# Performance work log

Measured on AMD Instinct MI355X. Metric: run time of the kernel, lower is better.

Reference implementation:

```python
import jax, jax.numpy as jnp
import numpy as np

B, N, DIM, H, DH = 8, 1024, 512, 8, 64
SCALE = DH ** -0.5
EPS = 1e-6


def setup_inputs() -> dict:
    key = jax.random.key(0)
    k1, k2, k3, k4 = jax.random.split(key, 4)
    x = jax.random.normal(k1, (B, N, DIM), dtype=jnp.float32)
    policy = (jax.random.uniform(k2, (B, N, 1)) < 0.7).astype(jnp.float32)
    W_qkv = jax.random.normal(k3, (DIM, 3 * H * DH), dtype=jnp.float32) * 0.02
    W_out = jax.random.normal(k4, (H * DH, DIM), dtype=jnp.float32) * 0.02
    b_out = jnp.zeros((DIM,), dtype=jnp.float32)
    return {"x": x, "policy": policy, "W_qkv": W_qkv, "W_out": W_out, "b_out": b_out}


def _softmax_with_policy(attn, policy, eps=EPS):
    # attn: [B,H,N,N], policy: [B,N,1]
    b, n = policy.shape[0], policy.shape[1]
    ap = policy.reshape(b, 1, 1, n)
    eye = jnp.eye(n, dtype=ap.dtype)[None, None]          # [1,1,N,N]
    ap = ap + (1.0 - ap) * eye                             # always attend to self
    max_att = jnp.max(attn, axis=-1, keepdims=True)
    e = jnp.exp(attn - max_att) * ap
    return (e + eps / n) / (jnp.sum(e, axis=-1, keepdims=True) + eps)


def reference(x, policy, W_qkv, W_out, b_out):
    qkv = x @ W_qkv                                        # [B,N,3*H*DH]
    q, k, v = jnp.split(qkv, 3, axis=-1)
    def to_heads(t):
        return t.reshape(B, N, H, DH).transpose(0, 2, 1, 3)  # [B,H,N,DH]
    q, k, v = to_heads(q), to_heads(k), to_heads(v)
    dots0 = jnp.einsum('bhid,bhjd->bhij', q, k) * SCALE    # [B,H,N,N]
    # NOTE: source computes relative-position bias in the rpe branch but never
    # adds it to dots (dead code); faithful output uses dots0 directly.
    attn = _softmax_with_policy(dots0, policy)
    out = jnp.einsum('bhij,bhjd->bhid', attn, v)           # [B,H,N,DH]
    out = out.transpose(0, 2, 1, 3).reshape(B, N, H * DH)  # [B,N,H*DH]
    out = out @ W_out + b_out                              # [B,N,DIM]
    return out, jax.nn.softmax(dots0, axis=-1)
```

## Files before the change

kernel.cpp:

```cpp
#include <hip/hip_runtime.h>

#define B_ 8
#define N_ 1024
#define DIM_ 512
#define H_ 8
#define DH_ 64
#define SCALE_ 0.125f
#define EPS_ 1e-6f
#define EPSN_ (1e-6f / 1024.0f)
#define C2_ (0.125f * 1.4426950408889634f)

typedef unsigned short u16;
typedef unsigned int u32;
typedef __attribute__((ext_vector_type(8))) short short8;
typedef __attribute__((ext_vector_type(8))) unsigned short ushort8;
typedef __attribute__((ext_vector_type(4))) unsigned short ushort4v;
typedef __attribute__((ext_vector_type(2))) unsigned int uint2v;
typedef __attribute__((ext_vector_type(4))) float f32x4;

__device__ __forceinline__ u16 f2b(float f) {
    union { float f; unsigned u; } v; v.f = f;
    unsigned r = v.u + 0x7fffu + ((v.u >> 16) & 1u);
    return (u16)(r >> 16);
}

__device__ __forceinline__ u32 cvtpk(float lo, float hi) {
    u32 r;
    asm("v_cvt_pk_bf16_f32 %0, %1, %2" : "=v"(r) : "v"(lo), "v"(hi));
    return r;
}

__device__ __forceinline__ f32x4 mfma16(short8 a, short8 b, f32x4 c) {
    return __builtin_amdgcn_mfma_f32_16x16x32_bf16(a, b, c, 0, 0, 0);
}

__device__ __forceinline__ void gload16(const u16* g, u16* l) {
    __builtin_amdgcn_global_load_lds(
        (const __attribute__((address_space(1))) void*)g,
        (__attribute__((address_space(3))) void*)l, 16, 0, 0);
}

#define WAITB(n) do {                                         \
    asm volatile("s_waitcnt vmcnt(" #n ")" ::: "memory");     \
    __builtin_amdgcn_s_barrier();                             \
    asm volatile("" ::: "memory");                            \
} while (0)

#define ENDB do {                                             \
    asm volatile("" ::: "memory");                            \
    __builtin_amdgcn_s_barrier();                             \
} while (0)

__global__ __launch_bounds__(256) void prep(
    const float* __restrict__ W_qkv, const float* __restrict__ W_out,
    const float* __restrict__ x,
    u16* __restrict__ wqkvT, u16* __restrict__ woutT, u16* __restrict__ Xb) {
    __shared__ float tl[64][65];
    const int t = threadIdx.x;
    const int blk = blockIdx.x;
    if (blk < 256) {
        const float* in; u16* out; int R, C, bx, by;
        if (blk < 192) { in = W_qkv; out = wqkvT; R = 512; C = 1536; bx = blk % 24; by = blk / 24; }
        else           { in = W_out; out = woutT; R = 512; C = 512;  bx = (blk - 192) & 7; by = (blk - 192) >> 3; }
        const int r0 = by * 64, c0 = bx * 64;
        const int rsub = t >> 6, col = t & 63;
#pragma unroll
        for (int k = 0; k < 16; ++k) {
            int row = k * 4 + rsub;
            tl[row][col] = in[(size_t)(r0 + row) * C + c0 + col];
        }
        __syncthreads();
#pragma unroll
        for (int k = 0; k < 16; ++k) {
            int orow = k * 4 + rsub;
            int ocol = col;
            out[(size_t)(c0 + orow) * R + r0 + ocol] = f2b(tl[ocol][orow]);
        }
    } else {
        int i2 = (blk - 256) * 2048 + t * 8;
        float4 f0 = *(const float4*)(x + i2);
        float4 f1 = *(const float4*)(x + i2 + 4);
        ushort8 o;
        o[0]=f2b(f0.x); o[1]=f2b(f0.y); o[2]=f2b(f0.z); o[3]=f2b(f0.w);
        o[4]=f2b(f1.x); o[5]=f2b(f1.y); o[6]=f2b(f1.z); o[7]=f2b(f1.w);
        *(ushort8*)(Xb + i2) = o;
    }
}

#define GSTAGE(buf, k0) do {                                                  \
    _Pragma("unroll")                                                         \
    for (int call = 0; call < 4; ++call) {                                    \
        const int rr2 = call * 32 + srow;                                     \
        gload16(Xb + (size_t)(rowbase + rr2) * DIM_ + (k0) + sch * 8,         \
                Alf + (buf) * 8192 + call * 2048 + t * 8);                    \
        gload16(BT + (size_t)(colbase + rr2) * DIM_ + (k0) + sch * 8,         \
                Blf + (buf) * 8192 + call * 2048 + t * 8);                    \
    }                                                                         \
} while (0)

#define QCOMP(bsel) do {                                                      \
    _Pragma("unroll")                                                         \
    for (int kk = 0; kk < 64; kk += 32) {                                     \
        short8 af[4], bf[4];                                                  \
        _Pragma("unroll")                                                     \
        for (int m = 0; m < 4; ++m) {                                         \
            const int ar = wr * 64 + m * 16 + lr;                             \
            const int slot = ((kk >> 3) + lg) ^ (lr & 7);                     \
            af[m] = *(const short8*)&Alf[(bsel) * 8192 + ar * 64 + slot * 8]; \
        }                                                                     \
        _Pragma("unroll")                                                     \
        for (int n = 0; n < 4; ++n) {                                         \
            const int br = wc * 64 + n * 16 + lr;                             \
            const int slot = ((kk >> 3) + lg) ^ (lr & 7);                     \
            bf[n] = *(const short8*)&Blf[(bsel) * 8192 + br * 64 + slot * 8]; \
        }                                                                     \
        _Pragma("unroll")                                                     \
        for (int m = 0; m < 4; ++m)                                           \
            _Pragma("unroll")                                                 \
            for (int n = 0; n < 4; ++n)                                       \
                acc[m][n] = mfma16(af[m], bf[n], acc[m][n]);                  \
    }                                                                         \
} while (0)

#define GEMM_PIPE do {                                                        \
    GSTAGE(0, 0);                                                             \
    GSTAGE(1, 64);  WAITB(8); QCOMP(0); ENDB;                                 \
    GSTAGE(0, 128); WAITB(8); QCOMP(1); ENDB;                                 \
    GSTAGE(1, 192); WAITB(8); QCOMP(0); ENDB;                                 \
    GSTAGE(0, 256); WAITB(8); QCOMP(1); ENDB;                                 \
    GSTAGE(1, 320); WAITB(8); QCOMP(0); ENDB;                                 \
    GSTAGE(0, 384); WAITB(8); QCOMP(1); ENDB;                                 \
    GSTAGE(1, 448); WAITB(8); QCOMP(0); ENDB;                                 \
    WAITB(0); QCOMP(1);                                                       \
} while (0)

__global__ __launch_bounds__(256, 2) void gemm_qkv(
    const u16* __restrict__ Xb, const u16* __restrict__ BT,
    u16* __restrict__ Qw, u16* __restrict__ Kw, u16* __restrict__ Vt) {
    __shared__ u16 Al[2 * 8192];
    __shared__ u16 Bl[2 * 8192];
    u16* Alf = &Al[0];
    u16* Blf = &Bl[0];
    const int t = threadIdx.x;
    const int w = t >> 6, l = t & 63, lg = l >> 4, lr = l & 15;
    const int wr = w >> 1, wc = w & 1;
    const int rowbase = blockIdx.y * 128, colbase = blockIdx.x * 128;
    const int srow = t >> 3;
    const int sch = (t & 7) ^ (srow & 7);

    f32x4 acc[4][4];
#pragma unroll
    for (int m = 0; m < 4; m++)
#pragma unroll
        for (int n = 0; n < 4; n++) acc[m][n] = (f32x4){0.f, 0.f, 0.f, 0.f};

    GEMM_PIPE;

#pragma unroll
    for (int m = 0; m < 4; m++) {
#pragma unroll
        for (int n = 0; n < 4; n++) {
#pragma unroll
            for (int j = 0; j < 4; j++) {
                int token = rowbase + wr * 64 + m * 16 + 4 * lg + j;
                int b = token >> 10, nn = token & (N_ - 1);
                int c = colbase + wc * 64 + n * 16 + lr;
                u16 v = f2b(acc[m][n][j]);
                if (c < 512) {
                    int h = c >> 6, d = c & 63;
                    Qw[((size_t)(b * H_ + h) * N_ + nn) * DH_ + d] = v;
                } else if (c < 1024) {
                    int c2 = c - 512, h = c2 >> 6, d = c2 & 63;
                    Kw[((size_t)(b * H_ + h) * N_ + nn) * DH_ + d] = v;
                } else {
                    int c2 = c - 1024, h = c2 >> 6, d = c2 & 63;
                    Vt[((size_t)(b * H_ + h) * DH_ + d) * N_ + nn] = v;
                }
            }
        }
    }
}

__global__ __launch_bounds__(256, 2) void gemm_out(
    const u16* __restrict__ Xb, const u16* __restrict__ BT,
    const float* __restrict__ bout, float* __restrict__ out) {
    __shared__ u16 Al[2 * 8192];
    __shared__ u16 Bl[2 * 8192];
    u16* Alf = &Al[0];
    u16* Blf = &Bl[0];
    const int t = threadIdx.x;
    const int w = t >> 6, l = t & 63, lg = l >> 4, lr = l & 15;
    const int wr = w >> 1, wc = w & 1;
    const int rowbase = blockIdx.y * 128, colbase = blockIdx.x * 128;
    const int srow = t >> 3;
    const int sch = (t & 7) ^ (srow & 7);

    f32x4 acc[4][4];
#pragma unroll
    for (int m = 0; m < 4; m++)
#pragma unroll
        for (int n = 0; n < 4; n++) acc[m][n] = (f32x4){0.f, 0.f, 0.f, 0.f};

    GEMM_PIPE;

#pragma unroll
    for (int n = 0; n < 4; n++) {
        const int cc = colbase + wc * 64 + n * 16 + lr;
        const float bv = bout[cc];
#pragma unroll
        for (int m = 0; m < 4; m++) {
#pragma unroll
            for (int j = 0; j < 4; j++) {
                int token = rowbase + wr * 64 + m * 16 + 4 * lg + j;
                out[(size_t)token * DIM_ + cc] = acc[m][n][j] + bv;
            }
        }
    }
}

#define STAGE_K2(c2) do {                                                     \
    gload16(Kb + ((size_t)((c2) * 128 + srow_)) * 64 + sch_ * 8,              \
            SH + ((c2) & 1) * 8192 + t * 8);                                  \
    gload16(Kb + ((size_t)((c2) * 128 + 64 + srow_)) * 64 + sch_ * 8,         \
            SH + ((c2) & 1) * 8192 + 4096 + t * 8);                           \
} while (0)

#define SUM128(c2) do {                                                       \
    _Pragma("unroll")                                                         \
    for (int sub = 0; sub < 8; ++sub) {                                       \
        const u16* kb = SH + ((c2) & 1) * 8192 + (sub >> 2) * 4096            \
                        + ((sub & 3) * 16 + lr) * 64;                         \
        short8 kf0 = *(const short8*)(kb + kswz);                             \
        short8 kf1 = *(const short8*)(kb + (kswz ^ 32));                      \
        f32x4 d = {0.f, 0.f, 0.f, 0.f};                                       \
        d = mfma16(kf0, qf0, d);                                              \
        d = mfma16(kf1, qf1, d);                                              \
        const int kb2 = (c2) * 128 + sub * 16 + 4 * lg;                       \
        f32x4 m4 = *(const f32x4*)&maskL[kb2];                                \
        _Pragma("unroll")                                                     \
        for (int j = 0; j < 4; ++j) {                                         \
            float E = __builtin_amdgcn_exp2f(d[j] * C2_);                     \
            float mm = (kb2 + j == q) ? 1.f : m4[j];                          \
            sp += E;                                                          \
            so = fmaf(E, mm, so);                                             \
        }                                                                     \
    }                                                                         \
} while (0)

#define STAGE_K(c) gload16(Kb + ((size_t)((c) * 64 + srow_)) * 64 + sch_ * 8, \
                           SH + ((c) & 1) * 4096 + t * 8)
#define STAGE_V(c) gload16(Vb + (size_t)srow_ * N_ + (c) * 64 + sch_ * 8,     \
                           SH + 8192 + ((c) & 1) * 4096 + t * 8)

#define QKTILE(c) do {                                                        \
    _Pragma("unroll")                                                         \
    for (int sub = 0; sub < 4; ++sub) {                                       \
        const u16* kb = SH + ((c) & 1) * 4096 + (sub * 16 + lr) * 64;         \
        short8 kf0 = *(const short8*)(kb + kswz);                             \
        short8 kf1 = *(const short8*)(kb + (kswz ^ 32));                      \
        f32x4 d = {0.f, 0.f, 0.f, 0.f};                                       \
        d = mfma16(kf0, qf0, d);                                              \
        d = mfma16(kf1, qf1, d);                                              \
        const int kb2 = (c) * 64 + sub * 16 + 4 * lg;                         \
        f32x4 m4 = *(const f32x4*)&maskL[kb2];                                \
        f32x4 ov; float p[4];                                                 \
        _Pragma("unroll")                                                     \
        for (int j = 0; j < 4; ++j) {                                         \
            float E = __builtin_amdgcn_exp2f(d[j] * C2_);                     \
            ov[j] = E * rip;                                                  \
            float mm = (kb2 + j == q) ? 1.f : m4[j];                          \
            p[j] = fmaf(E * mm, rpo, eb);                                     \
        }                                                                     \
        uint2v wv2;                                                           \
        wv2[0] = cvtpk(p[0], p[1]);                                           \
        wv2[1] = cvtpk(p[2], p[3]);                                           \
        *(f32x4*)(srow + (c) * 64 + sub * 16 + 4 * lg) = ov;                  \
        *(uint2v*)&wl[wid][lr][sub * 16 + 4 * lg] = wv2;                      \
    }                                                                         \
} while (0)

#define PVTILE(c) do {                                                        \
    __builtin_amdgcn_s_setprio(1);                                            \
    _Pragma("unroll")                                                         \
    for (int ks = 0; ks < 64; ks += 32) {                                     \
        short8 af = *(const short8*)&wl[wid][lr][ks + 8 * lg];                \
        _Pragma("unroll")                                                     \
        for (int dt = 0; dt < 4; ++dt) {                                      \
            const u16* vb = SH + 8192 + ((c) & 1) * 4096 + (dt * 16 + lr) * 64; \
            short8 vf = *(const short8*)(vb + (ks ? (kswz ^ 32) : kswz));     \
            apv[dt] = mfma16(af, vf, apv[dt]);                                \
        }                                                                     \
    }                                                                         \
    __builtin_amdgcn_s_setprio(0);                                            \
} while (0)

__global__ __launch_bounds__(512, 2) void attn_kernel(
    const u16* __restrict__ Qw, const u16* __restrict__ Kw, const u16* __restrict__ Vt,
    const float* __restrict__ policy, u16* __restrict__ outpre, float* __restrict__ softout) {
    __shared__ u16 SH[16384];
    __shared__ u16 wl[8][16][72];
    __shared__ float maskL[N_];

    const int t = threadIdx.x;
    const int wid = t >> 6, l = t & 63, lg = (l >> 4), lr = l & 15;
    const int srow_ = t >> 3, sch_ = (t & 7) ^ ((t >> 3) & 7);
    const int kswz = (lg ^ (lr & 7)) * 8;

    const int bid = blockIdx.x;
    const int xcd = bid & 7, rr = bid >> 3;
    const int g = rr >> 3, rt = rr & 7;
    const int bh = g * 8 + xcd;
    const int b = bh >> 3, h = bh & 7;
    const int n0 = rt * 128 + wid * 16;
    const int q = n0 + lr;

    const u16* Qb = Qw + ((size_t)bh * N_ + n0) * DH_;
    const u16* Kb = Kw + (size_t)bh * N_ * DH_;
    const u16* Vb = Vt + (size_t)bh * DH_ * N_;
    const float* pol = policy + b * N_;

    short8 qf0 = *(const short8*)(Qb + lr * DH_ + 8 * lg);
    short8 qf1 = *(const short8*)(Qb + lr * DH_ + 32 + 8 * lg);

    {
        float2 pv = *(const float2*)(pol + t * 2);
        maskL[t * 2 + 0] = pv.x > 0.5f ? 1.f : 0.f;
        maskL[t * 2 + 1] = pv.y > 0.5f ? 1.f : 0.f;
    }
    __syncthreads();

    float sp = 0.f, so = 0.f;
    STAGE_K2(0);
#define ITER1(c2, n) do { STAGE_K2(n); WAITB(2); SUM128(c2); ENDB; } while (0)
    ITER1(0, 1); ITER1(1, 2); ITER1(2, 3); ITER1(3, 4);
    ITER1(4, 5); ITER1(5, 6); ITER1(6, 7);
    WAITB(0); SUM128(7); ENDB;

    sp += __shfl_xor(sp, 16); sp += __shfl_xor(sp, 32);
    so += __shfl_xor(so, 16); so += __shfl_xor(so, 32);
    const float rip = 1.f / sp;
    const float rpo = 1.f / (so + EPS_);
    const float eb = EPSN_ * rpo;

    f32x4 apv[4];
#pragma unroll
    for (int i = 0; i < 4; i++) apv[i] = (f32x4){0, 0, 0, 0};
    float* srow = softout + ((size_t)bh * N_ + q) * N_;

    STAGE_K(0); STAGE_V(0);
    STAGE_K(1); STAGE_V(1); WAITB(2); QKTILE(0); PVTILE(0); ENDB;
#define ITER2(c, n) do { STAGE_K(n); STAGE_V(n); WAITB(6); QKTILE(c); PVTILE(c); ENDB; } while (0)
    ITER2(1, 2);  ITER2(2, 3);  ITER2(3, 4);  ITER2(4, 5);
    ITER2(5, 6);  ITER2(6, 7);  ITER2(7, 8);  ITER2(8, 9);
    ITER2(9, 10); ITER2(10, 11); ITER2(11, 12); ITER2(12, 13);
    ITER2(13, 14); ITER2(14, 15);
    WAITB(4); QKTILE(15); PVTILE(15);

#pragma unroll
    for (int dt = 0; dt < 4; dt++) {
#pragma unroll
        for (int j = 0; j < 4; j++) {
            outpre[(size_t)(b * N_ + n0 + 4 * lg + j) * DIM_ + h * DH_ + dt * 16 + lr]
                = f2b(apv[dt][j]);
        }
    }
}

extern "C" void kernel_launch(void* const* d_in, const int* in_sizes, int n_in,
                              void* d_out, int out_size, void* d_ws, size_t ws_size,
                              hipStream_t stream) {
    const float* x      = (const float*)d_in[0];
    const float* policy = (const float*)d_in[1];
    const float* W_qkv  = (const float*)d_in[2];
    const float* W_out  = (const float*)d_in[3];
    const float* b_out  = (const float*)d_in[4];
    float* out = (float*)d_out;
    float* softout = out + (size_t)B_ * N_ * DIM_;

    char* ws = (char*)d_ws;
    u16* wqkvT = (u16*)ws;
    u16* woutT = (u16*)(ws + 1572864);
    u16* Xb    = (u16*)(ws + 2097152);
    u16* Qw    = (u16*)(ws + 10485760);
    u16* Kw    = (u16*)(ws + 18874368);
    u16* Vt    = (u16*)(ws + 27262976);
    u16* pre   = (u16*)(ws + 35651584);

    prep<<<2304, 256, 0, stream>>>(W_qkv, W_out, x, wqkvT, woutT, Xb);
    gemm_qkv<<<dim3(12, 64), 256, 0, stream>>>(Xb, wqkvT, Qw, Kw, Vt);
    attn_kernel<<<512, 512, 0, stream>>>(Qw, Kw, Vt, policy, pre, softout);
    gemm_out<<<dim3(4, 64), 256, 0, stream>>>(pre, woutT, b_out, out);
}
```

Baseline: 141.6 us.

## Triple-buffer K/V shared-memory staging and drop per-iteration end barriers

Switches the K and V LDS staging from double to triple buffering (indices mod 3) and enlarges shared memory to fit. Loads for tile n+2 are issued before computing tile n, and the trailing per-iteration barrier is removed, so each iteration needs only one wait/barrier. The aim is to hide global-load latency and cut synchronisation. In exchange LDS use rises, which may limit occupancy at 2 blocks per CU, and the buffer-reuse safety now depends on the new wait-count sequencing.

```diff
diff --git a/kernel.cpp b/kernel.cpp
--- a/kernel.cpp
+++ b/kernel.cpp
@@ -220,15 +220,15 @@
 
 #define STAGE_K2(c2) do {                                                     \
     gload16(Kb + ((size_t)((c2) * 128 + srow_)) * 64 + sch_ * 8,              \
-            SH + ((c2) & 1) * 8192 + t * 8);                                  \
+            SH + ((c2) % 3) * 8192 + t * 8);                                  \
     gload16(Kb + ((size_t)((c2) * 128 + 64 + srow_)) * 64 + sch_ * 8,         \
-            SH + ((c2) & 1) * 8192 + 4096 + t * 8);                           \
+            SH + ((c2) % 3) * 8192 + 4096 + t * 8);                           \
 } while (0)
 
 #define SUM128(c2) do {                                                       \
     _Pragma("unroll")                                                         \
     for (int sub = 0; sub < 8; ++sub) {                                       \
-        const u16* kb = SH + ((c2) & 1) * 8192 + (sub >> 2) * 4096            \
+        const u16* kb = SH + ((c2) % 3) * 8192 + (sub >> 2) * 4096            \
                         + ((sub & 3) * 16 + lr) * 64;                         \
         short8 kf0 = *(const short8*)(kb + kswz);                             \
         short8 kf1 = *(const short8*)(kb + (kswz ^ 32));                      \
@@ -248,14 +248,14 @@
 } while (0)
 
 #define STAGE_K(c) gload16(Kb + ((size_t)((c) * 64 + srow_)) * 64 + sch_ * 8, \
-                           SH + ((c) & 1) * 4096 + t * 8)
+                           SH + ((c) % 3) * 4096 + t * 8)
 #define STAGE_V(c) gload16(Vb + (size_t)srow_ * N_ + (c) * 64 + sch_ * 8,     \
-                           SH + 8192 + ((c) & 1) * 4096 + t * 8)
+                           SH + 12288 + ((c) % 3) * 4096 + t * 8)
 
 #define QKTILE(c) do {                                                        \
     _Pragma("unroll")                                                         \
     for (int sub = 0; sub < 4; ++sub) {                                       \
-        const u16* kb = SH + ((c) & 1) * 4096 + (sub * 16 + lr) * 64;         \
+        const u16* kb = SH + ((c) % 3) * 4096 + (sub * 16 + lr) * 64;         \
         short8 kf0 = *(const short8*)(kb + kswz);                             \
         short8 kf1 = *(const short8*)(kb + (kswz ^ 32));                      \
         f32x4 d = {0.f, 0.f, 0.f, 0.f};                                       \
@@ -286,7 +286,7 @@
         short8 af = *(const short8*)&wl[wid][lr][ks + 8 * lg];                \
         _Pragma("unroll")                                                     \
         for (int dt = 0; dt < 4; ++dt) {                                      \
-            const u16* vb = SH + 8192 + ((c) & 1) * 4096 + (dt * 16 + lr) * 64; \
+            const u16* vb = SH + 12288 + ((c) % 3) * 4096 + (dt * 16 + lr) * 64; \
             short8 vf = *(const short8*)(vb + (ks ? (kswz ^ 32) : kswz));     \
             apv[dt] = mfma16(af, vf, apv[dt]);                                \
         }                                                                     \
@@ -297,7 +297,7 @@
 __global__ __launch_bounds__(512, 2) void attn_kernel(
     const u16* __restrict__ Qw, const u16* __restrict__ Kw, const u16* __restrict__ Vt,
     const float* __restrict__ policy, u16* __restrict__ outpre, float* __restrict__ softout) {
-    __shared__ u16 SH[16384];
+    __shared__ u16 SH[24576];
     __shared__ u16 wl[8][16][72];
     __shared__ float maskL[N_];
 
@@ -330,11 +330,16 @@
     __syncthreads();
 
     float sp = 0.f, so = 0.f;
-    STAGE_K2(0);
-#define ITER1(c2, n) do { STAGE_K2(n); WAITB(2); SUM128(c2); ENDB; } while (0)
-    ITER1(0, 1); ITER1(1, 2); ITER1(2, 3); ITER1(3, 4);
-    ITER1(4, 5); ITER1(5, 6); ITER1(6, 7);
-    WAITB(0); SUM128(7); ENDB;
+    STAGE_K2(0); STAGE_K2(1);
+    WAITB(2); STAGE_K2(2); SUM128(0);
+    WAITB(2); STAGE_K2(3); SUM128(1);
+    WAITB(2); STAGE_K2(4); SUM128(2);
+    WAITB(2); STAGE_K2(5); SUM128(3);
+    WAITB(2); STAGE_K2(6); SUM128(4);
+    WAITB(2); STAGE_K2(7); SUM128(5);
+    WAITB(2); SUM128(6);
+    WAITB(0); SUM128(7);
+    ENDB;
 
     sp += __shfl_xor(sp, 16); sp += __shfl_xor(sp, 32);
     so += __shfl_xor(so, 16); so += __shfl_xor(so, 32);
@@ -347,14 +352,15 @@
     for (int i = 0; i < 4; i++) apv[i] = (f32x4){0, 0, 0, 0};
     float* srow = softout + ((size_t)bh * N_ + q) * N_;
 
-    STAGE_K(0); STAGE_V(0);
-    STAGE_K(1); STAGE_V(1); WAITB(2); QKTILE(0); PVTILE(0); ENDB;
-#define ITER2(c, n) do { STAGE_K(n); STAGE_V(n); WAITB(6); QKTILE(c); PVTILE(c); ENDB; } while (0)
-    ITER2(1, 2);  ITER2(2, 3);  ITER2(3, 4);  ITER2(4, 5);
-    ITER2(5, 6);  ITER2(6, 7);  ITER2(7, 8);  ITER2(8, 9);
-    ITER2(9, 10); ITER2(10, 11); ITER2(11, 12); ITER2(12, 13);
-    ITER2(13, 14); ITER2(14, 15);
-    WAITB(4); QKTILE(15); PVTILE(15);
+    STAGE_K(0); STAGE_V(0); STAGE_K(1); STAGE_V(1);
+    WAITB(2); STAGE_K(2); STAGE_V(2); QKTILE(0); PVTILE(0);
+    WAITB(6); STAGE_K(3); STAGE_V(3); QKTILE(1); PVTILE(1);
+#define P2(c, n) do { WAITB(10); STAGE_K(n); STAGE_V(n); QKTILE(c); PVTILE(c); } while (0)
+    P2(2, 4);  P2(3, 5);  P2(4, 6);  P2(5, 7);
+    P2(6, 8);  P2(7, 9);  P2(8, 10); P2(9, 11);
+    P2(10, 12); P2(11, 13); P2(12, 14); P2(13, 15);
+    WAITB(10); QKTILE(14); PVTILE(14);
+    WAITB(8); QKTILE(15); PVTILE(15);
 
 #pragma unroll
     for (int dt = 0; dt < 4; dt++) {
```

New measurement: 153.5 us. +8.4%, slower.
